# Performance work log

Hardware: AMD Instinct MI355X
Metric: run time of the kernel (lower is better)

Reference implementation:

```python
import jax, jax.numpy as jnp
import numpy as np

D_IN = 1024
D_STATE = 1024
B = 128
L = 512


def _linear(x, W, b):
    # torch nn.Linear convention: W is (out, in)
    return x @ W.T + b


def setup_inputs() -> dict:
    key = jax.random.key(0)
    ks = jax.random.split(key, 11)
    s = 0.02
    past = jax.random.normal(ks[0], (B, L, D_IN), dtype=jnp.float32)
    # init_proj: Linear(d_in, d_state) -> SiLU -> Linear(d_state, d_state)
    Wi1 = jax.random.normal(ks[1], (D_STATE, D_IN), jnp.float32) * s
    bi1 = jnp.zeros((D_STATE,), jnp.float32)
    Wi2 = jax.random.normal(ks[2], (D_STATE, D_STATE), jnp.float32) * s
    bi2 = jnp.zeros((D_STATE,), jnp.float32)
    # transition: Linear(d_state+d_in, 2*d_state) -> SiLU -> Linear(2*d_state, d_state) -> SiLU -> Linear(d_state, d_state)
    Wt1 = jax.random.normal(ks[3], (2 * D_STATE, D_STATE + D_IN), jnp.float32) * s
    bt1 = jnp.zeros((2 * D_STATE,), jnp.float32)
    Wt2 = jax.random.normal(ks[4], (D_STATE, 2 * D_STATE), jnp.float32) * s
    bt2 = jnp.zeros((D_STATE,), jnp.float32)
    Wt3 = jax.random.normal(ks[5], (D_STATE, D_STATE), jnp.float32) * s
    bt3 = jnp.zeros((D_STATE,), jnp.float32)
    return {
        "past": past,
        "Wi1": Wi1, "bi1": bi1, "Wi2": Wi2, "bi2": bi2,
        "Wt1": Wt1, "bt1": bt1, "Wt2": Wt2, "bt2": bt2,
        "Wt3": Wt3, "bt3": bt3,
    }


def reference(past, Wi1, bi1, Wi2, bi2, Wt1, bt1, Wt2, bt2, Wt3, bt3):
    # s0 = init_proj(past[:, 0, :])
    h0 = jax.nn.silu(_linear(past[:, 0, :], Wi1, bi1))
    s0 = _linear(h0, Wi2, bi2)  # (B, d_state)

    def step(s_prev, x_t):
        h = jnp.concatenate([s_prev, x_t], axis=-1)  # (B, d_state + d_in)
        h = jax.nn.silu(_linear(h, Wt1, bt1))        # (B, 2*d_state)
        h = jax.nn.silu(_linear(h, Wt2, bt2))        # (B, d_state)
        s = _linear(h, Wt3, bt3)                     # (B, d_state)
        return s, s

    xs = jnp.swapaxes(past[:, 1:, :], 0, 1)          # (L-1, B, d_in)
    _, states_rest = jax.lax.scan(step, s0, xs)      # (L-1, B, d_state)
    states = jnp.concatenate([s0[None], states_rest], axis=0)  # (L, B, d_state)
    return jnp.swapaxes(states, 0, 1)                # (B, L, d_state)
```

## Files before the change

### kernel.cpp

```cpp
#include <hip/hip_runtime.h>
#include <hip/hip_bf16.h>


typedef __bf16 v8bf __attribute__((ext_vector_type(8)));
typedef float f32x4 __attribute__((ext_vector_type(4)));
typedef unsigned u32x4 __attribute__((ext_vector_type(4)));

#define REP1 (128 * 2048)
#define REP2 (128 * 1024)

__device__ inline f32x4 mfma16(v8bf a, v8bf b, f32x4 c) {
  return __builtin_amdgcn_mfma_f32_16x16x32_bf16(a, b, c, 0, 0, 0);
}
__device__ inline float silu_f(float x) { return x / (1.f + __expf(-x)); }
__device__ inline v8bf as8(f32x4 x) { union { f32x4 f; v8bf b; } u; u.f = x; return u.b; }
__device__ inline v8bf cvt8(float4 a, float4 b) {
  v8bf v;
  v[0] = (__bf16)a.x; v[1] = (__bf16)a.y; v[2] = (__bf16)a.z; v[3] = (__bf16)a.w;
  v[4] = (__bf16)b.x; v[5] = (__bf16)b.y; v[6] = (__bf16)b.z; v[7] = (__bf16)b.w;
  return v;
}
__device__ inline unsigned bfb(float v) {
  __bf16 b = (__bf16)v; unsigned short u; __builtin_memcpy(&u, &b, 2); return (unsigned)u;
}

#define CLOADP(dst, base, boff)                                        \
  asm volatile("global_load_dwordx4 %0, %1, off offset:%2"             \
               : "=v"(dst) : "v"(base), "n"(boff))
#define CLOADC(dst, base)                                              \
  asm volatile("global_load_dwordx4 %0, %1, off sc0 sc1" : "=v"(dst) : "v"(base))

template <int N> __device__ inline void vwait() {
  asm volatile("s_waitcnt vmcnt(%0)" :: "n"(N) : "memory");
  __builtin_amdgcn_sched_barrier(0);
}
__device__ inline void vwait_n(int n) {
  switch (n) {
    case 0: vwait<0>(); break;   case 1: vwait<1>(); break;
    case 2: vwait<2>(); break;   case 3: vwait<3>(); break;
    case 4: vwait<4>(); break;   case 5: vwait<5>(); break;
    case 6: vwait<6>(); break;   case 7: vwait<7>(); break;
    case 8: vwait<8>(); break;   case 9: vwait<9>(); break;
    case 10: vwait<10>(); break; case 11: vwait<11>(); break;
    case 12: vwait<12>(); break; case 13: vwait<13>(); break;
    case 14: vwait<14>(); break; default: vwait<15>(); break;
  }
}

__device__ inline void poll32(const unsigned* f, unsigned tgt, int* dead) {
  if (threadIdx.x < 8 && !*dead) {
    const unsigned* p = f + threadIdx.x * 4;
    int guard = 0;
    while (true) {
      u32x4 v;
      asm volatile("global_load_dwordx4 %0, %1, off sc0 sc1\n\ts_waitcnt vmcnt(0)"
                   : "=v"(v) : "v"(p) : "memory");
      if (v[0] >= tgt && v[1] >= tgt && v[2] >= tgt && v[3] >= tgt) break;
      if (++guard > (1 << 18)) { *dead = 1; break; }
      __builtin_amdgcn_s_sleep(1);
    }
  }
  __syncthreads();
}
__device__ inline void release(unsigned* f, int slot, unsigned v) {
  asm volatile("s_waitcnt vmcnt(0)" ::: "memory");
  __syncthreads();
  if (threadIdx.x == 0)
    asm volatile("global_store_dword %0, %1, off sc0 sc1" :: "v"(f + slot), "v"(v) : "memory");
}

__global__ void cvt_kernel(const float* __restrict__ src, __bf16* __restrict__ dst,
                           int total8, int log2cols, int sstride, int soff) {
  int i = blockIdx.x * 256 + threadIdx.x;
  if (i >= total8) return;
  long long e = (long long)i * 8;
  int r = (int)(e >> log2cols);
  int c = (int)(e & ((1LL << log2cols) - 1));
  const float* s = src + (size_t)r * sstride + soff + c;
  float4 f0 = *(const float4*)(s);
  float4 f1 = *(const float4*)(s + 4);
  *(v8bf*)(dst + e) = cvt8(f0, f1);
}

__global__ void tpose_kernel(const float* __restrict__ src, __bf16* __restrict__ dst,
                             int R, int C) {
  __shared__ float tile[32][33];
  const int tid = threadIdx.x;
  const int r0 = blockIdx.y * 32, c0 = blockIdx.x * 32;
  const int lr = tid >> 5, lc = tid & 31;
#pragma unroll
  for (int p = 0; p < 4; ++p)
    tile[lr + p * 8][lc] = src[(size_t)(r0 + lr + p * 8) * C + c0 + lc];
  __syncthreads();
#pragma unroll
  for (int p = 0; p < 4; ++p)
    dst[(size_t)(c0 + lr + p * 8) * R + r0 + lc] = (__bf16)tile[lc][lr + p * 8];
}

__global__ __launch_bounds__(256, 1) void comp_gemm_kernel(
    const __bf16* __restrict__ A, const __bf16* __restrict__ B,
    __bf16* __restrict__ out) {
  const int tid = threadIdx.x, wid = tid >> 6, lane = tid & 63;
  const int lr = lane & 15, lc = lane >> 4;
  const int m0 = blockIdx.x * 32;
  const int c0 = blockIdx.y * 128 + wid * 32;
  const __bf16* ap0 = A + (size_t)(m0 + lr) * 1024 + lc * 8;
  const __bf16* ap1 = ap0 + (size_t)16 * 1024;
  const __bf16* bp = B + (size_t)(c0 + lr) * 1024 + lc * 8;
  f32x4 acc[2][2] = {};
#pragma unroll 8
  for (int k = 0; k < 1024; k += 32) {
    v8bf a0 = *(const v8bf*)(ap0 + k);
    v8bf a1 = *(const v8bf*)(ap1 + k);
#pragma unroll
    for (int f = 0; f < 2; ++f) {
      v8bf b = *(const v8bf*)(bp + (size_t)f * 16 * 1024 + k);
      acc[0][f] = mfma16(a0, b, acc[0][f]);
      acc[1][f] = mfma16(a1, b, acc[1][f]);
    }
  }
  const int cm = lc << 2, cn = lr;
#pragma unroll
  for (int mf = 0; mf < 2; ++mf)
#pragma unroll
    for (int f = 0; f < 2; ++f)
#pragma unroll
      for (int r = 0; r < 4; ++r)
        out[(size_t)(m0 + mf * 16 + cm + r) * 1024 + c0 + f * 16 + cn] =
            (__bf16)acc[mf][f][r];
}

__global__ void bias_comp_kernel(const float* __restrict__ Wt1,
                                 const float* __restrict__ bt3,
                                 const float* __restrict__ bi2,
                                 float* __restrict__ b13, float* __restrict__ b1i2) {
  const int n = blockIdx.x * 4 + (threadIdx.x >> 6);
  const int lane = threadIdx.x & 63;
  const float* row = Wt1 + (size_t)n * 2048;
  float v1 = 0.f, v2 = 0.f;
#pragma unroll
  for (int i = 0; i < 16; ++i) {
    int k = lane + i * 64;
    float w = row[k];
    v1 += w * bt3[k];
    v2 += w * bi2[k];
  }
  for (int o = 32; o; o >>= 1) { v1 += __shfl_down(v1, o); v2 += __shfl_down(v2, o); }
  if (lane == 0) { b13[n] = v1; b1i2[n] = v2; }
}

__global__ __launch_bounds__(512, 1) void xc_gemm_kernel(
    const float* __restrict__ past, const __bf16* __restrict__ w1x,
    const float* __restrict__ bt1, __bf16* __restrict__ xc) {
  const int t = blockIdx.z + 1;
  const int mh = blockIdx.y;
  const int nb = blockIdx.x;
  const int tid = threadIdx.x, wid = tid >> 6, lane = tid & 63;
  const int wm = wid >> 2, wn = wid & 3;
  const int m0 = mh * 64 + wm * 32;
  const int n0 = nb * 512 + wn * 128;
  const int lr = lane & 15, lc = lane >> 4;
  f32x4 acc[2][8] = {};
  const float* a0p = past + ((size_t)(m0 + lr) * 512 + t) * 1024 + lc * 8;
  const float* a1p = a0p + (size_t)16 * 512 * 1024;
  const __bf16* bp = w1x + (size_t)(n0 + lr) * 1024 + lc * 8;
#pragma unroll 4
  for (int k = 0; k < 1024; k += 32) {
    float4 x00 = *(const float4*)(a0p + k);
    float4 x01 = *(const float4*)(a0p + k + 4);
    float4 x10 = *(const float4*)(a1p + k);
    float4 x11 = *(const float4*)(a1p + k + 4);
    v8bf a0 = cvt8(x00, x01), a1 = cvt8(x10, x11);
#pragma unroll
    for (int j = 0; j < 8; ++j) {
      v8bf b = *(const v8bf*)(bp + (size_t)j * 16 * 1024 + k);
      acc[0][j] = mfma16(a0, b, acc[0][j]);
      acc[1][j] = mfma16(a1, b, acc[1][j]);
    }
  }
  const int cm = lc << 2, cn = lr;
#pragma unroll
  for (int f = 0; f < 2; ++f)
#pragma unroll
    for (int j = 0; j < 8; ++j) {
      int n = n0 + j * 16 + cn;
      float bias = bt1[n];
#pragma unroll
      for (int r = 0; r < 4; ++r) {
        int m = m0 + f * 16 + cm + r;
        xc[((size_t)m * 512 + t) * 2048 + n] = (__bf16)(acc[f][j][r] + bias);
      }
    }
}

template <int K>
__device__ inline void stage_issue(f32x4* v, const __bf16* src, int tid) {
  constexpr int KC = K / 8;
#pragma unroll
  for (int i = 0; i < K / 128; ++i) {
    int idx = tid + i * 256;
    int row = idx / KC, kc = idx % KC;
    CLOADC(v[i], src + (size_t)row * K + kc * 8);
  }
}
template <int K>
__device__ inline void stage_commit(char* lds, f32x4* v, int tid) {
  constexpr int KC = K / 8;
#pragma unroll
  for (int i = 0; i < K / 128; ++i) {
    int idx = tid + i * 256;
    int row = idx / KC, kc = idx % KC;
    unsigned byte = ((unsigned)(row * K + kc * 8) * 2) ^ ((unsigned)(row & 7) << 4);
    *(f32x4*)(lds + byte) = v[i];
  }
  __syncthreads();
}

template <int KIT, int PFD, int KSB>
__device__ inline f32x4 ring_run1(const char* ldsa, int k0, const __bf16* wtb,
                                  f32x4 (&rw)[PFD], int lane) {
  const int lr = lane & 15, lc = lane >> 4;
  f32x4 acc = {0.f, 0.f, 0.f, 0.f};
#pragma unroll
  for (int it = 0; it < KIT; ++it) {
    vwait_n((KIT - 1 - it) < (PFD - 1) ? (KIT - 1 - it) : (PFD - 1));
    v8bf b = as8(rw[it % PFD]);
    if (it + PFD < KIT) CLOADP(rw[it % PFD], wtb, (it + PFD) * 64);
    int k = k0 + it * 32 + lc * 8;
    unsigned byte = ((unsigned)(lr * KSB + k) * 2) ^ ((unsigned)(lr & 7) << 4);
    v8bf a = *(const v8bf*)(ldsa + byte);
    acc = mfma16(a, b, acc);
  }
  return acc;
}
template <int PFD>
__device__ inline void ring_pre(const __bf16* wtb, f32x4 (&rw)[PFD]) {
#pragma unroll
  for (int j = 0; j < PFD; ++j) CLOADP(rw[j], wtb, j * 64);
}

__device__ inline f32x4 gemm_aa16(const char* ldsa, int k0, const char* ldsw,
                                  int kb0, int col, int lane) {
  const int lr = lane & 15, lc = lane >> 4;
  f32x4 acc = {0.f, 0.f, 0.f, 0.f};
#pragma unroll
  for (int it = 0; it < 16; ++it) {
    int k = k0 + it * 32 + lc * 8;
    unsigned abyte = ((unsigned)(lr * 1024 + k) * 2) ^ ((unsigned)(lr & 7) << 4);
    v8bf a = *(const v8bf*)(ldsa + abyte);
    v8bf b = *(const v8bf*)(ldsw + (size_t)((kb0 + it * 4 + lc) * 32 + col) * 16);
    acc = mfma16(a, b, acc);
  }
  return acc;
}

__global__ __launch_bounds__(256, 1) void recurrent_kernel(
    const __bf16* __restrict__ wWi1, const __bf16* __restrict__ wWi2,
    const __bf16* __restrict__ wW13, const __bf16* __restrict__ wW1i2,
    const __bf16* __restrict__ wWt2, const __bf16* __restrict__ wWt3,
    const __bf16* __restrict__ x0bf,
    __bf16* __restrict__ z1, __bf16* __restrict__ z2,
    const float* __restrict__ bi1, const float* __restrict__ bi2,
    const float* __restrict__ bt2, const float* __restrict__ bt3,
    const float* __restrict__ b13, const float* __restrict__ b1i2,
    float* __restrict__ out, unsigned* __restrict__ flags) {
  __shared__ alignas(16) char actbuf[65536];
  __shared__ alignas(16) char wt3buf[65536];
  __shared__ alignas(16) char scratch[4096];
  __shared__ int s_dead;
  const int bid = blockIdx.x;
  const int g = bid >> 5, s = bid & 31;
  const int tid = threadIdx.x, wid = tid >> 6, lane = tid & 63;
  const int lr = lane & 15, lc = lane >> 4;
  const int cm = lc << 2, cn = lr;
  const int wn = wid & 1, wk = wid >> 1;
  const int b0 = g * 16;
  const int rp = s & 3;
  if (tid == 0) s_dead = 0;

  unsigned* fA = flags + g * 64;
  unsigned* fB = fA + 32;
  const __bf16* xc = (const __bf16*)out;
  __bf16* tposeb = (__bf16*)scratch;
  float* red = (float*)scratch;
  float* fin = (float*)(scratch + 2048);

  {
    const __bf16* wg = wWt3 + (size_t)s * 32 * 1024;
    for (int idx = tid; idx < 4096; idx += 256) {
      int kb = idx >> 5, c = idx & 31;
      *(f32x4*)(wt3buf + (size_t)idx * 16) = *(const f32x4*)(wg + (size_t)c * 1024 + kb * 8);
    }
  }

  const int nBC = s * 32 + wn * 16 + cn;
  const int nA = s * 64 + wid * 16 + cn;
  const float bB = bt2[nBC], bCt = bt3[nBC];
  const float bI1 = bi1[nBC], bC0 = bi2[nBC];
  const float bA13 = b13[nA], bA1i2 = b1i2[nA];

  auto storeZ2 = [&](__bf16* base) {
    int row = tid >> 4, col = (tid * 2) & 31;
    unsigned d = bfb(fin[row * 32 + col]) | (bfb(fin[row * 32 + col + 1]) << 16);
#pragma unroll
    for (int rep = 0; rep < 4; ++rep) {
      __bf16* p = base + (size_t)rep * REP2 + (size_t)(b0 + row) * 1024 + s * 32 + col;
      asm volatile("global_store_dword %0, %1, off sc0 sc1" :: "v"(p), "v"(d) : "memory");
    }
  };
  auto storeOut = [&](int tt) {
    int row = tid >> 4, col = (tid * 2) & 31;
    float2 o; o.x = fin[row * 32 + col]; o.y = fin[row * 32 + col + 1];
    *(float2*)(out + (size_t)(b0 + row) * 524288 + (size_t)tt * 1024 + s * 32 + col) = o;
  };

  {
    f32x4 sv[8];
    stage_issue<1024>(sv, x0bf + (size_t)b0 * 1024, tid);
    f32x4 rw[8];
    const __bf16* wtb = wWi1 + (size_t)(nBC - cn + lr) * 1024 + wk * 512 + lc * 8;
    ring_pre<8>(wtb, rw);
    vwait<0>();
    stage_commit<1024>(actbuf, sv, tid);
    f32x4 acc = ring_run1<16, 8, 1024>(actbuf, wk * 512, wtb, rw, lane);
    if (wk) {
#pragma unroll
      for (int r = 0; r < 4; ++r) red[wn * 256 + (cm + r) * 16 + cn] = acc[r];
    }
    __syncthreads();
    if (!wk) {
#pragma unroll
      for (int r = 0; r < 4; ++r)
        fin[(cm + r) * 32 + wn * 16 + cn] =
            silu_f(acc[r] + red[wn * 256 + (cm + r) * 16 + cn] + bI1);
    }
    __syncthreads();
    storeZ2(z2);
    release(fB, s, 1u);
  }

  for (int t = 1; t < 512; ++t) {
    {
      const __bf16* wtbA = (t == 1 ? wW1i2 : wW13) +
                           (size_t)(s * 64 + wid * 16 + lr) * 1024 + lc * 8;
      const float bAv = (t == 1) ? bA1i2 : bA13;
      unsigned xcu[4];
#pragma unroll
      for (int r = 0; r < 4; ++r) {
        const __bf16* p = xc + ((size_t)(b0 + cm + r) * 512 + t) * 2048 + nA;
        asm volatile("global_load_ushort %0, %1, off sc0 sc1" : "=v"(xcu[r]) : "v"(p));
      }
      f32x4 rw[16];
      ring_pre<16>(wtbA, rw);
      poll32(fB, (unsigned)t, &s_dead);
      f32x4 sv[8];
      stage_issue<1024>(sv, z2 + ((size_t)((t - 1) & 1) * 4 + rp) * REP2 +
                                (size_t)b0 * 1024, tid);
      vwait<0>();
      stage_commit<1024>(actbuf, sv, tid);
      f32x4 acc = ring_run1<32, 16, 1024>(actbuf, 0, wtbA, rw, lane);
#pragma unroll
      for (int r = 0; r < 4; ++r) {
        float xv = __uint_as_float(xcu[r] << 16);
        tposeb[(cm + r) * 64 + wid * 16 + cn] = (__bf16)silu_f(acc[r] + xv + bAv);
      }
      __syncthreads();
      {
        int row = tid >> 4, col = (tid * 4) & 63;
        unsigned long long d = *(const unsigned long long*)(tposeb + row * 64 + col);
#pragma unroll
        for (int rep = 0; rep < 4; ++rep) {
          __bf16* p = z1 + (size_t)rep * REP1 + (size_t)(b0 + row) * 2048 + s * 64 + col;
          asm volatile("global_store_dwordx2 %0, %1, off sc0 sc1" :: "v"(p), "v"(d) : "memory");
        }
      }
      release(fA, s, (unsigned)t);
    }
    {
      f32x4 acc;
      if (t == 1) {
        const __bf16* wtbC = wWi2 + (size_t)(nBC - cn + lr) * 1024 + wk * 512 + lc * 8;
        f32x4 rw[8];
        ring_pre<8>(wtbC, rw);
        acc = ring_run1<16, 8, 1024>(actbuf, wk * 512, wtbC, rw, lane);
      } else {
        acc = gemm_aa16(actbuf, wk * 512, wt3buf, wk * 64, wn * 16 + lr, lane);
      }
      const float bCv = (t == 1) ? bC0 : bCt;
      if (wk) {
#pragma unroll
        for (int r = 0; r < 4; ++r) red[wn * 256 + (cm + r) * 16 + cn] = acc[r];
      }
      __syncthreads();
      if (!wk) {
#pragma unroll
        for (int r = 0; r < 4; ++r)
          fin[(cm + r) * 32 + wn * 16 + cn] =
              acc[r] + red[wn * 256 + (cm + r) * 16 + cn] + bCv;
      }
      __syncthreads();
      storeOut(t - 1);
    }
    {
      const __bf16* wtbB = wWt2 + (size_t)(nBC - cn + lr) * 2048 + wk * 1024 + lc * 8;
      f32x4 rw[16];
      ring_pre<16>(wtbB, rw);
      poll32(fA, (unsigned)t, &s_dead);
      f32x4 sv[16];
      stage_issue<2048>(sv, z1 + (size_t)rp * REP1 + (size_t)b0 * 2048, tid);
      vwait<0>();
      stage_commit<2048>(actbuf, sv, tid);
      f32x4 acc = ring_run1<32, 16, 2048>(actbuf, wk * 1024, wtbB, rw, lane);
      if (wk) {
#pragma unroll
        for (int r = 0; r < 4; ++r) red[wn * 256 + (cm + r) * 16 + cn] = acc[r];
      }
      __syncthreads();
      if (!wk) {
#pragma unroll
        for (int r = 0; r < 4; ++r)
          fin[(cm + r) * 32 + wn * 16 + cn] =
              silu_f(acc[r] + red[wn * 256 + (cm + r) * 16 + cn] + bB);
      }
      __syncthreads();
      storeZ2(z2 + (size_t)(t & 1) * 4 * REP2);
      release(fB, s, (unsigned)(t + 1));
    }
  }
  {
    poll32(fB, 512u, &s_dead);
    f32x4 sv[8];
    stage_issue<1024>(sv, z2 + ((size_t)1 * 4 + rp) * REP2 + (size_t)b0 * 1024, tid);
    vwait<0>();
    stage_commit<1024>(actbuf, sv, tid);
    f32x4 acc = gemm_aa16(actbuf, wk * 512, wt3buf, wk * 64, wn * 16 + lr, lane);
    if (wk) {
#pragma unroll
      for (int r = 0; r < 4; ++r) red[wn * 256 + (cm + r) * 16 + cn] = acc[r];
    }
    __syncthreads();
    if (!wk) {
#pragma unroll
      for (int r = 0; r < 4; ++r)
        fin[(cm + r) * 32 + wn * 16 + cn] =
            acc[r] + red[wn * 256 + (cm + r) * 16 + cn] + bCt;
    }
    __syncthreads();
    storeOut(511);
  }
}

extern "C" void kernel_launch(void* const* d_in, const int* in_sizes, int n_in,
                              void* d_out, int out_size, void* d_ws, size_t ws_size,
                              hipStream_t stream) {
  (void)in_sizes; (void)n_in; (void)out_size; (void)ws_size;
  const float* past = (const float*)d_in[0];
  const float* Wi1 = (const float*)d_in[1];
  const float* bi1 = (const float*)d_in[2];
  const float* Wi2 = (const float*)d_in[3];
  const float* bi2 = (const float*)d_in[4];
  const float* Wt1 = (const float*)d_in[5];
  const float* bt1 = (const float*)d_in[6];
  const float* Wt2 = (const float*)d_in[7];
  const float* bt2 = (const float*)d_in[8];
  const float* Wt3 = (const float*)d_in[9];
  const float* bt3 = (const float*)d_in[10];
  float* out = (float*)d_out;

  char* ws = (char*)d_ws;
  size_t off = 0;
  unsigned* flags = (unsigned*)(ws + off); off += 4096;
  __bf16* wWi1 = (__bf16*)(ws + off);  off += (size_t)1024 * 1024 * 2;
  __bf16* wWi2 = (__bf16*)(ws + off);  off += (size_t)1024 * 1024 * 2;
  __bf16* wWt1s = (__bf16*)(ws + off); off += (size_t)2048 * 1024 * 2;
  __bf16* wWt1x = (__bf16*)(ws + off); off += (size_t)2048 * 1024 * 2;
  __bf16* wWt2 = (__bf16*)(ws + off);  off += (size_t)1024 * 2048 * 2;
  __bf16* wWt3 = (__bf16*)(ws + off);  off += (size_t)1024 * 1024 * 2;
  __bf16* wWt3T = (__bf16*)(ws + off); off += (size_t)1024 * 1024 * 2;
  __bf16* wWi2T = (__bf16*)(ws + off); off += (size_t)1024 * 1024 * 2;
  __bf16* wW13 = (__bf16*)(ws + off);  off += (size_t)2048 * 1024 * 2;
  __bf16* wW1i2 = (__bf16*)(ws + off); off += (size_t)2048 * 1024 * 2;
  float* b13 = (float*)(ws + off);     off += 2048 * 4;
  float* b1i2 = (float*)(ws + off);    off += 2048 * 4;
  __bf16* x0bf = (__bf16*)(ws + off);  off += (size_t)128 * 1024 * 2;
  __bf16* z1 = (__bf16*)(ws + off);    off += (size_t)4 * REP1 * 2;
  __bf16* z2 = (__bf16*)(ws + off);    off += (size_t)8 * REP2 * 2;

  hipMemsetAsync(flags, 0, 4096, stream);

  auto cvt = [&](const float* s, __bf16* d, int rows, int cols, int log2c,
                 int sstride, int soff) {
    int total8 = rows * cols / 8;
    cvt_kernel<<<dim3((total8 + 255) / 256), dim3(256), 0, stream>>>(
        s, d, total8, log2c, sstride, soff);
  };
  cvt(Wi1, wWi1, 1024, 1024, 10, 1024, 0);
  cvt(Wi2, wWi2, 1024, 1024, 10, 1024, 0);
  cvt(Wt1, wWt1s, 2048, 1024, 10, 2048, 0);
  cvt(Wt1, wWt1x, 2048, 1024, 10, 2048, 1024);
  cvt(Wt2, wWt2, 1024, 2048, 11, 2048, 0);
  cvt(Wt3, wWt3, 1024, 1024, 10, 1024, 0);
  cvt(past, x0bf, 128, 1024, 10, 512 * 1024, 0);

  tpose_kernel<<<dim3(32, 32), dim3(256), 0, stream>>>(Wt3, wWt3T, 1024, 1024);
  tpose_kernel<<<dim3(32, 32), dim3(256), 0, stream>>>(Wi2, wWi2T, 1024, 1024);
  comp_gemm_kernel<<<dim3(64, 8), dim3(256), 0, stream>>>(wWt1s, wWt3T, wW13);
  comp_gemm_kernel<<<dim3(64, 8), dim3(256), 0, stream>>>(wWt1s, wWi2T, wW1i2);
  bias_comp_kernel<<<dim3(512), dim3(256), 0, stream>>>(Wt1, bt3, bi2, b13, b1i2);

  xc_gemm_kernel<<<dim3(4, 2, 511), dim3(512), 0, stream>>>(
      past, wWt1x, bt1, (__bf16*)d_out);

  recurrent_kernel<<<dim3(256), dim3(256), 0, stream>>>(
      wWi1, wWi2, wW13, wW1i2, wWt2, wWt3, x0bf, z1, z2,
      bi1, bi2, bt2, bt3, b13, b1i2, out, flags);
}
```

Baseline: 8.006 ms.

## Pre-convert past to bf16 for xc GEMM and drop replicated z1/z2 stores

```diff
diff --git a/kernel.cpp b/kernel.cpp
--- a/kernel.cpp
+++ b/kernel.cpp
@@ -149,8 +149,9 @@
   if (lane == 0) { b13[n] = v1; b1i2[n] = v2; }
 }
 
+template <bool BF16A>
 __global__ __launch_bounds__(512, 1) void xc_gemm_kernel(
-    const float* __restrict__ past, const __bf16* __restrict__ w1x,
+    const void* __restrict__ pastv, const __bf16* __restrict__ w1x,
     const float* __restrict__ bt1, __bf16* __restrict__ xc) {
   const int t = blockIdx.z + 1;
   const int mh = blockIdx.y;
@@ -161,21 +162,39 @@
   const int n0 = nb * 512 + wn * 128;
   const int lr = lane & 15, lc = lane >> 4;
   f32x4 acc[2][8] = {};
-  const float* a0p = past + ((size_t)(m0 + lr) * 512 + t) * 1024 + lc * 8;
-  const float* a1p = a0p + (size_t)16 * 512 * 1024;
   const __bf16* bp = w1x + (size_t)(n0 + lr) * 1024 + lc * 8;
+  if constexpr (BF16A) {
+    const __bf16* a0p = (const __bf16*)pastv +
+                        ((size_t)(m0 + lr) * 512 + t) * 1024 + lc * 8;
+    const __bf16* a1p = a0p + (size_t)16 * 512 * 1024;
 #pragma unroll 4
-  for (int k = 0; k < 1024; k += 32) {
-    float4 x00 = *(const float4*)(a0p + k);
-    float4 x01 = *(const float4*)(a0p + k + 4);
-    float4 x10 = *(const float4*)(a1p + k);
-    float4 x11 = *(const float4*)(a1p + k + 4);
-    v8bf a0 = cvt8(x00, x01), a1 = cvt8(x10, x11);
-#pragma unroll
-    for (int j = 0; j < 8; ++j) {
-      v8bf b = *(const v8bf*)(bp + (size_t)j * 16 * 1024 + k);
-      acc[0][j] = mfma16(a0, b, acc[0][j]);
-      acc[1][j] = mfma16(a1, b, acc[1][j]);
+    for (int k = 0; k < 1024; k += 32) {
+      v8bf a0 = *(const v8bf*)(a0p + k);
+      v8bf a1 = *(const v8bf*)(a1p + k);
+#pragma unroll
+      for (int j = 0; j < 8; ++j) {
+        v8bf b = *(const v8bf*)(bp + (size_t)j * 16 * 1024 + k);
+        acc[0][j] = mfma16(a0, b, acc[0][j]);
+        acc[1][j] = mfma16(a1, b, acc[1][j]);
+      }
+    }
+  } else {
+    const float* a0p = (const float*)pastv +
+                       ((size_t)(m0 + lr) * 512 + t) * 1024 + lc * 8;
+    const float* a1p = a0p + (size_t)16 * 512 * 1024;
+#pragma unroll 4
+    for (int k = 0; k < 1024; k += 32) {
+      float4 x00 = *(const float4*)(a0p + k);
+      float4 x01 = *(const float4*)(a0p + k + 4);
+      float4 x10 = *(const float4*)(a1p + k);
+      float4 x11 = *(const float4*)(a1p + k + 4);
+      v8bf a0 = cvt8(x00, x01), a1 = cvt8(x10, x11);
+#pragma unroll
+      for (int j = 0; j < 8; ++j) {
+        v8bf b = *(const v8bf*)(bp + (size_t)j * 16 * 1024 + k);
+        acc[0][j] = mfma16(a0, b, acc[0][j]);
+        acc[1][j] = mfma16(a1, b, acc[1][j]);
+      }
     }
   }
   const int cm = lc << 2, cn = lr;
@@ -275,7 +294,6 @@
   const int cm = lc << 2, cn = lr;
   const int wn = wid & 1, wk = wid >> 1;
   const int b0 = g * 16;
-  const int rp = s & 3;
   if (tid == 0) s_dead = 0;
 
   unsigned* fA = flags + g * 64;
@@ -302,11 +320,8 @@
   auto storeZ2 = [&](__bf16* base) {
     int row = tid >> 4, col = (tid * 2) & 31;
     unsigned d = bfb(fin[row * 32 + col]) | (bfb(fin[row * 32 + col + 1]) << 16);
-#pragma unroll
-    for (int rep = 0; rep < 4; ++rep) {
-      __bf16* p = base + (size_t)rep * REP2 + (size_t)(b0 + row) * 1024 + s * 32 + col;
-      asm volatile("global_store_dword %0, %1, off sc0 sc1" :: "v"(p), "v"(d) : "memory");
-    }
+    __bf16* p = base + (size_t)(b0 + row) * 1024 + s * 32 + col;
+    asm volatile("global_store_dword %0, %1, off sc0 sc1" :: "v"(p), "v"(d) : "memory");
   };
   auto storeOut = [&](int tt) {
     int row = tid >> 4, col = (tid * 2) & 31;
@@ -354,8 +369,7 @@
       ring_pre<16>(wtbA, rw);
       poll32(fB, (unsigned)t, &s_dead);
       f32x4 sv[8];
-      stage_issue<1024>(sv, z2 + ((size_t)((t - 1) & 1) * 4 + rp) * REP2 +
-                                (size_t)b0 * 1024, tid);
+      stage_issue<1024>(sv, z2 + (size_t)((t - 1) & 1) * REP2 + (size_t)b0 * 1024, tid);
       vwait<0>();
       stage_commit<1024>(actbuf, sv, tid);
       f32x4 acc = ring_run1<32, 16, 1024>(actbuf, 0, wtbA, rw, lane);
@@ -368,11 +382,8 @@
       {
         int row = tid >> 4, col = (tid * 4) & 63;
         unsigned long long d = *(const unsigned long long*)(tposeb + row * 64 + col);
-#pragma unroll
-        for (int rep = 0; rep < 4; ++rep) {
-          __bf16* p = z1 + (size_t)rep * REP1 + (size_t)(b0 + row) * 2048 + s * 64 + col;
-          asm volatile("global_store_dwordx2 %0, %1, off sc0 sc1" :: "v"(p), "v"(d) : "memory");
-        }
+        __bf16* p = z1 + (size_t)(b0 + row) * 2048 + s * 64 + col;
+        asm volatile("global_store_dwordx2 %0, %1, off sc0 sc1" :: "v"(p), "v"(d) : "memory");
       }
       release(fA, s, (unsigned)t);
     }
@@ -407,7 +418,7 @@
       ring_pre<16>(wtbB, rw);
       poll32(fA, (unsigned)t, &s_dead);
       f32x4 sv[16];
-      stage_issue<2048>(sv, z1 + (size_t)rp * REP1 + (size_t)b0 * 2048, tid);
+      stage_issue<2048>(sv, z1 + (size_t)b0 * 2048, tid);
       vwait<0>();
       stage_commit<2048>(actbuf, sv, tid);
       f32x4 acc = ring_run1<32, 16, 2048>(actbuf, wk * 1024, wtbB, rw, lane);
@@ -423,14 +434,14 @@
               silu_f(acc[r] + red[wn * 256 + (cm + r) * 16 + cn] + bB);
       }
       __syncthreads();
-      storeZ2(z2 + (size_t)(t & 1) * 4 * REP2);
+      storeZ2(z2 + (size_t)(t & 1) * REP2);
       release(fB, s, (unsigned)(t + 1));
     }
   }
   {
     poll32(fB, 512u, &s_dead);
     f32x4 sv[8];
-    stage_issue<1024>(sv, z2 + ((size_t)1 * 4 + rp) * REP2 + (size_t)b0 * 1024, tid);
+    stage_issue<1024>(sv, z2 + (size_t)1 * REP2 + (size_t)b0 * 1024, tid);
     vwait<0>();
     stage_commit<1024>(actbuf, sv, tid);
     f32x4 acc = gemm_aa16(actbuf, wk * 512, wt3buf, wk * 64, wn * 16 + lr, lane);
@@ -453,7 +464,7 @@
 extern "C" void kernel_launch(void* const* d_in, const int* in_sizes, int n_in,
                               void* d_out, int out_size, void* d_ws, size_t ws_size,
                               hipStream_t stream) {
-  (void)in_sizes; (void)n_in; (void)out_size; (void)ws_size;
+  (void)in_sizes; (void)n_in; (void)out_size;
   const float* past = (const float*)d_in[0];
   const float* Wi1 = (const float*)d_in[1];
   const float* bi1 = (const float*)d_in[2];
@@ -483,14 +494,17 @@
   float* b13 = (float*)(ws + off);     off += 2048 * 4;
   float* b1i2 = (float*)(ws + off);    off += 2048 * 4;
   __bf16* x0bf = (__bf16*)(ws + off);  off += (size_t)128 * 1024 * 2;
-  __bf16* z1 = (__bf16*)(ws + off);    off += (size_t)4 * REP1 * 2;
-  __bf16* z2 = (__bf16*)(ws + off);    off += (size_t)8 * REP2 * 2;
+  __bf16* z1 = (__bf16*)(ws + off);    off += (size_t)REP1 * 2;
+  __bf16* z2 = (__bf16*)(ws + off);    off += (size_t)2 * REP2 * 2;
+  __bf16* pbf = (__bf16*)(ws + off);
+  const size_t need_pbf = off + (size_t)128 * 512 * 1024 * 2;
+  const bool use_pbf = ws_size >= need_pbf;
 
   hipMemsetAsync(flags, 0, 4096, stream);
 
-  auto cvt = [&](const float* s, __bf16* d, int rows, int cols, int log2c,
+  auto cvt = [&](const float* s, __bf16* d, size_t rows, int cols, int log2c,
                  int sstride, int soff) {
-    int total8 = rows * cols / 8;
+    int total8 = (int)(rows * (size_t)cols / 8);
     cvt_kernel<<<dim3((total8 + 255) / 256), dim3(256), 0, stream>>>(
         s, d, total8, log2c, sstride, soff);
   };
@@ -508,8 +522,14 @@
   comp_gemm_kernel<<<dim3(64, 8), dim3(256), 0, stream>>>(wWt1s, wWi2T, wW1i2);
   bias_comp_kernel<<<dim3(512), dim3(256), 0, stream>>>(Wt1, bt3, bi2, b13, b1i2);
 
-  xc_gemm_kernel<<<dim3(4, 2, 511), dim3(512), 0, stream>>>(
-      past, wWt1x, bt1, (__bf16*)d_out);
+  if (use_pbf) {
+    cvt(past, pbf, (size_t)128 * 512, 1024, 10, 1024, 0);
+    xc_gemm_kernel<true><<<dim3(4, 2, 511), dim3(512), 0, stream>>>(
+        pbf, wWt1x, bt1, (__bf16*)d_out);
+  } else {
+    xc_gemm_kernel<false><<<dim3(4, 2, 511), dim3(512), 0, stream>>>(
+        past, wWt1x, bt1, (__bf16*)d_out);
+  }
 
   recurrent_kernel<<<dim3(256), dim3(256), 0, stream>>>(
       wWi1, wWi2, wW13, wW1i2, wWt2, wWt3, x0bf, z1, z2,
```

Result: faster. 7.541 ms (-5.8%).
